# Kernel tuning notes

Measured on AMD Instinct MI355X. Metric: run time of the kernel, lower is better.

The kernel has to match this reference:

```python
import jax, jax.numpy as jnp
import numpy as np

N = 100000   # nodes
E = 800000   # edges per layer
H = 4        # heads
C = 32       # per-head channels (hidden_channels // heads)
IN = 128
HID = H * C  # 128
NEG_SLOPE = 0.2


def gat_layer(x, edge_index, W, att_src, att_dst, bias):
    # PyG GATConv (concat=True, add_self_loops=True)
    n = x.shape[0]
    loop = jnp.arange(n, dtype=edge_index.dtype)
    src = jnp.concatenate([edge_index[0], loop])
    dst = jnp.concatenate([edge_index[1], loop])
    h = (x @ W).reshape(n, H, C)                     # [N,H,C]
    a_src = jnp.sum(h * att_src, axis=-1)            # [N,H]
    a_dst = jnp.sum(h * att_dst, axis=-1)            # [N,H]
    e = jax.nn.leaky_relu(a_src[src] + a_dst[dst], NEG_SLOPE)  # [E',H]
    # segment softmax over incoming edges of each destination node
    m = jax.ops.segment_max(e, dst, num_segments=n)  # [N,H]
    e = jnp.exp(e - m[dst])
    s = jax.ops.segment_sum(e, dst, num_segments=n)  # [N,H]
    alpha = e / (s[dst] + 1e-16)                     # [E',H]
    msg = h[src] * alpha[:, :, None]                 # [E',H,C]
    out = jax.ops.segment_sum(msg, dst, num_segments=n)  # [N,H,C]
    return out.reshape(n, H * C) + bias


def setup_inputs() -> dict:
    key = jax.random.key(0)
    ks = jax.random.split(key, 20)
    inp = {"x": jax.random.normal(ks[0], (N, IN), jnp.float32)}
    dins = [IN, HID, HID]
    for l in range(3):
        din = dins[l]
        inp[f"edge_index{l}"] = jax.random.randint(ks[1 + l], (2, E), 0, N, dtype=jnp.int32)
        inp[f"W{l}"] = jax.random.normal(ks[4 + l], (din, H * C), jnp.float32) / np.sqrt(din)
        inp[f"att_src{l}"] = jax.random.normal(ks[7 + l], (H, C), jnp.float32) * 0.1
        inp[f"att_dst{l}"] = jax.random.normal(ks[10 + l], (H, C), jnp.float32) * 0.1
        inp[f"bias{l}"] = jnp.zeros((H * C,), jnp.float32)
    return inp


def reference(x, edge_index0, edge_index1, edge_index2,
              W0, att_src0, att_dst0, bias0,
              W1, att_src1, att_dst1, bias1,
              W2, att_src2, att_dst2, bias2):
    edges = [edge_index0, edge_index1, edge_index2]
    params = [(W0, att_src0, att_dst0, bias0),
              (W1, att_src1, att_dst1, bias1),
              (W2, att_src2, att_dst2, bias2)]
    for ei, (W, a_s, a_d, b) in zip(edges, params):
        x = jax.nn.relu(gat_layer(x, ei, W, a_s, a_d, b))
    return x
```

## Files before the change

kernel.cpp:

```cpp
#include <hip/hip_runtime.h>
#include <hip/hip_bf16.h>
#include <hip/hip_fp16.h>
#include <type_traits>

#define NNODES 100000
#define NEDGES 800000
#define HIDDIM 128
#define NHEAD 4

#define EPB 8192
#define NBLK 98
#define BSH 7
#define NBUCK 782

typedef _Float16 half8 __attribute__((ext_vector_type(8)));
typedef _Float16 half2t __attribute__((ext_vector_type(2)));
typedef float floatx4 __attribute__((ext_vector_type(4)));


__global__ __launch_bounds__(256) void bucketA_k(const int* __restrict__ e0,
                                                 const int* __restrict__ e1,
                                                 const int* __restrict__ e2,
                                                 int* __restrict__ counts) {
    __shared__ int hist[NBUCK];
    int l = blockIdx.y;
    const int* dst = ((l == 0) ? e0 : (l == 1) ? e1 : e2) + NEDGES;
    int j = blockIdx.x;
    for (int t = threadIdx.x; t < NBUCK; t += 256) hist[t] = 0;
    __syncthreads();
    int base = j * EPB;
    int lim = min(EPB, NEDGES - base);
    for (int i = threadIdx.x; i < lim; i += 256)
        atomicAdd(&hist[dst[base + i] >> BSH], 1);
    __syncthreads();
    int* crow = counts + ((size_t)l * NBLK + j) * NBUCK;
    for (int t = threadIdx.x; t < NBUCK; t += 256) crow[t] = hist[t];
}

__global__ __launch_bounds__(128) void bucketB1_k(int* __restrict__ counts,
                                                  int* __restrict__ bucketTotal) {
    __shared__ int sd[128];
    int b = blockIdx.x, l = blockIdx.y;
    int t = threadIdx.x;
    int v = (t < NBLK) ? counts[((size_t)l * NBLK + t) * NBUCK + b] : 0;
    sd[t] = v;
    __syncthreads();
    for (int off = 1; off < 128; off <<= 1) {
        int u = (t >= off) ? sd[t - off] : 0;
        __syncthreads();
        sd[t] += u;
        __syncthreads();
    }
    if (t < NBLK) counts[((size_t)l * NBLK + t) * NBUCK + b] = sd[t] - v;
    if (t == 127) bucketTotal[l * NBUCK + b] = sd[127];
}

__global__ __launch_bounds__(1024) void bucketB2_k(const int* __restrict__ bucketTotal,
                                                   int* __restrict__ ebBase,
                                                   int* __restrict__ csrBase) {
    __shared__ int sd[1024];
    int l = blockIdx.x;
    int t = threadIdx.x;
    int tot = (t < NBUCK) ? bucketTotal[l * NBUCK + t] : 0;
    sd[t] = tot;
    __syncthreads();
    for (int off = 1; off < 1024; off <<= 1) {
        int u = (t >= off) ? sd[t - off] : 0;
        __syncthreads();
        sd[t] += u;
        __syncthreads();
    }
    if (t < NBUCK) ebBase[l * NBUCK + t] = sd[t] - tot;
    __syncthreads();
    int nb = (t == NBUCK - 1) ? (NNODES - (NBUCK - 1) * 128) : 128;
    int v2 = (t < NBUCK) ? (tot + nb) : 0;
    sd[t] = v2;
    __syncthreads();
    for (int off = 1; off < 1024; off <<= 1) {
        int u = (t >= off) ? sd[t - off] : 0;
        __syncthreads();
        sd[t] += u;
        __syncthreads();
    }
    if (t < NBUCK) csrBase[l * NBUCK + t] = sd[t] - v2;
}

__global__ __launch_bounds__(256) void bucketC_k(const int* __restrict__ e0,
                                                 const int* __restrict__ e1,
                                                 const int* __restrict__ e2,
                                                 const int* __restrict__ counts,
                                                 const int* __restrict__ ebBase,
                                                 int* __restrict__ edgeBuf) {
    __shared__ int cur[NBUCK];
    int l = blockIdx.y;
    const int* ei = (l == 0) ? e0 : (l == 1) ? e1 : e2;
    const int* src = ei;
    const int* dst = ei + NEDGES;
    int j = blockIdx.x;
    const int* bs = counts + ((size_t)l * NBLK + j) * NBUCK;
    const int* eb = ebBase + l * NBUCK;
    for (int t = threadIdx.x; t < NBUCK; t += 256) cur[t] = eb[t] + bs[t];
    __syncthreads();
    int base = j * EPB;
    int lim = min(EPB, NEDGES - base);
    int* ebuf = edgeBuf + (size_t)l * NEDGES;
    for (int i = threadIdx.x; i < lim; i += 256) {
        int d = dst[base + i];
        int s = src[base + i];
        int pos = atomicAdd(&cur[d >> BSH], 1);
        ebuf[pos] = ((d & 127) << 17) | s;
    }
}

__global__ __launch_bounds__(256) void bucketD_k(const int* __restrict__ edgeBuf,
                                                 const int* __restrict__ bucketTotal,
                                                 const int* __restrict__ ebBase,
                                                 const int* __restrict__ csrBase,
                                                 int* __restrict__ offs,
                                                 int* __restrict__ deg,
                                                 int* __restrict__ srcs) {
    __shared__ int cnt[128];
    __shared__ int offl[128];
    __shared__ int cur[128];
    int b = blockIdx.x, l = blockIdx.y;
    int t = threadIdx.x;
    int nb = (b == NBUCK - 1) ? (NNODES - (NBUCK - 1) * 128) : 128;
    int eb0 = ebBase[l * NBUCK + b];
    int ecnt = bucketTotal[l * NBUCK + b];
    int csr0 = csrBase[l * NBUCK + b];
    const int* ebuf = edgeBuf + (size_t)l * NEDGES;
    int* srcsL = srcs + (size_t)l * (NEDGES + NNODES);
    if (t < 128) cnt[t] = 0;
    __syncthreads();
    for (int i = t; i < ecnt; i += 256)
        atomicAdd(&cnt[ebuf[eb0 + i] >> 17], 1);
    __syncthreads();
    if (t < 128) {
        int lane = t & 63;
        int x = cnt[t] + 1;
        #pragma unroll
        for (int o = 1; o < 64; o <<= 1) {
            int u = __shfl_up(x, o);
            if (lane >= o) x += u;
        }
        offl[t] = x;
    }
    __syncthreads();
    if (t < 128) {
        int c = cnt[t];
        int incl = offl[t] + ((t >= 64) ? offl[63] : 0);
        int o = csr0 + incl - (c + 1);
        cur[t] = o;
        if (t < nb) {
            int node = b * 128 + t;
            offs[l * NNODES + node] = o;
            deg[l * NNODES + node] = c;
            srcsL[o + c] = node;
        }
    }
    __syncthreads();
    for (int i = t; i < ecnt; i += 256) {
        int w = ebuf[eb0 + i];
        int pos = atomicAdd(&cur[w >> 17], 1);
        srcsL[pos] = w & 0x1FFFF;
    }
}


template <typename AT>
__global__ __launch_bounds__(256, 2) void gemm_mfma_k(const AT* __restrict__ A,
                                                      const float* __restrict__ B,
                                                      const float* __restrict__ attS,
                                                      const float* __restrict__ attD,
                                                      __half* __restrict__ C16,
                                                      float* __restrict__ aSD, int M) {
    __shared__ __half Bt[144 * 136];
    const int tid = threadIdx.x;
    {
        int kk = (tid & 63) * 2;
        int g = tid >> 6;
        #pragma unroll
        for (int jn = 0; jn < 8; jn++) {
            int n0 = g * 4 + jn * 16;
            float4 r0 = *(const float4*)(B + (size_t)kk * 128 + n0);
            float4 r1 = *(const float4*)(B + (size_t)(kk + 1) * 128 + n0);
            float f0[4] = {r0.x, r0.y, r0.z, r0.w};
            float f1[4] = {r1.x, r1.y, r1.z, r1.w};
            #pragma unroll
            for (int i = 0; i < 4; i++)
                *(__half2*)(&Bt[(n0 + i) * 136 + kk]) = __floats2half2_rn(f0[i], f1[i]);
        }
    }
    if (tid < 128) {
        int k = tid;
        const float* Brow = B + (size_t)k * 128;
        #pragma unroll
        for (int h = 0; h < NHEAD; h++) {
            float s0 = 0.f, s1 = 0.f;
            #pragma unroll 8
            for (int c = 0; c < 32; c++) {
                float bb = Brow[h * 32 + c];
                s0 += bb * attS[h * 32 + c];
                s1 += bb * attD[h * 32 + c];
            }
            Bt[(128 + h * 2 + 0) * 136 + k] = (_Float16)s0;
            Bt[(128 + h * 2 + 1) * 136 + k] = (_Float16)s1;
        }
    } else {
        int k = tid - 128;
        #pragma unroll
        for (int j = 8; j < 16; j++) Bt[(128 + j) * 136 + k] = (_Float16)0.f;
    }
    __syncthreads();

    const int lane = tid & 63;
    const int wave = tid >> 6;
    const int m = lane & 15;
    const int q = lane >> 4;

    half8 bfrag[9][4];
    #pragma unroll
    for (int c = 0; c < 9; c++)
        #pragma unroll
        for (int t = 0; t < 4; t++)
            bfrag[c][t] = *(const half8*)(&Bt[(c * 16 + m) * 136 + t * 32 + q * 8]);

    for (int iter = 0; iter < 4; iter++) {
        int rb = blockIdx.x * 256 + iter * 64 + wave * 16;
        if (rb >= M) break;
        int row = rb + m;
        int rowc = row < M ? row : M - 1;
        half8 a[4];
        if constexpr (std::is_same<AT, __half>::value) {
            const __half* ap = A + (size_t)rowc * HIDDIM;
            #pragma unroll
            for (int t = 0; t < 4; t++)
                a[t] = *(const half8*)(ap + t * 32 + q * 8);
        } else {
            const float* ap = A + (size_t)rowc * HIDDIM;
            #pragma unroll
            for (int t = 0; t < 4; t++) {
                float4 u = *(const float4*)(ap + t * 32 + q * 8);
                float4 v = *(const float4*)(ap + t * 32 + q * 8 + 4);
                half8 h;
                h[0] = (_Float16)u.x; h[1] = (_Float16)u.y;
                h[2] = (_Float16)u.z; h[3] = (_Float16)u.w;
                h[4] = (_Float16)v.x; h[5] = (_Float16)v.y;
                h[6] = (_Float16)v.z; h[7] = (_Float16)v.w;
                a[t] = h;
            }
        }
        floatx4 acc[9];
        #pragma unroll
        for (int c = 0; c < 9; c++) acc[c] = (floatx4){0.f, 0.f, 0.f, 0.f};
        #pragma unroll
        for (int t = 0; t < 4; t++)
            #pragma unroll
            for (int c = 0; c < 9; c++)
                acc[c] = __builtin_amdgcn_mfma_f32_16x16x32_f16(a[t], bfrag[c][t], acc[c], 0, 0, 0);
        #pragma unroll
        for (int c = 0; c < 8; c++)
            #pragma unroll
            for (int r = 0; r < 4; r++) {
                int grow = rb + q * 4 + r;
                if (grow < M)
                    C16[(size_t)grow * HIDDIM + c * 16 + m] = __float2half(acc[c][r]);
            }
        if (m < 8) {
            #pragma unroll
            for (int r = 0; r < 4; r++) {
                int grow = rb + q * 4 + r;
                if (grow < M) aSD[(size_t)grow * 8 + m] = acc[8][r];
            }
        }
    }
}


template <bool HALF_OUT>
__global__ __launch_bounds__(256) void agg_k(const __half* __restrict__ h16,
                                             const int* __restrict__ offs,
                                             const int* __restrict__ deg,
                                             const int* __restrict__ srcs,
                                             const float* __restrict__ aSD,
                                             const float* __restrict__ bias,
                                             void* __restrict__ outv) {
    int tid = threadIdx.x;
    int lane = tid & 63;
    int grp = lane >> 4;
    int cg = lane & 15;
    int c8 = cg * 8;
    int h2 = (cg >> 2) * 2;
    int n = blockIdx.x * 16 + (tid >> 6) * 4 + grp;
    bool nvalid = n < NNODES;
    int nn = nvalid ? n : NNODES - 1;
    int start = offs[nn];
    int cnt = deg[nn] + 1;
    float ad = aSD[(size_t)nn * 8 + h2 + 1];
    half2t acc0[4], acc1[4];
    #pragma unroll
    for (int i = 0; i < 4; i++) {
        acc0[i] = (half2t){(_Float16)0.f, (_Float16)0.f};
        acc1[i] = (half2t){(_Float16)0.f, (_Float16)0.f};
    }
    float wsum = 0.f;
    const int base = grp * 16;

    for (int chunk = 0; chunk < cnt; chunk += 16) {
        int idx = chunk + cg;
        int lim = min(16, cnt - chunk);
        int sv = srcs[start + (idx < cnt ? idx : cnt - 1)];
        int s_a = __shfl(sv, base + 0);
        int s_b = __shfl(sv, base + 1);
        float as_a = aSD[(size_t)s_a * 8 + h2];
        float as_b = aSD[(size_t)s_b * 8 + h2];
        half8 hv_a = *(const half8*)(h16 + (size_t)s_a * HIDDIM + c8);
        half8 hv_b = *(const half8*)(h16 + (size_t)s_b * HIDDIM + c8);
        for (int j = 0; j < lim; j += 2) {
            int j2 = (j + 2 < 16) ? j + 2 : 15;
            int j3 = (j + 3 < 16) ? j + 3 : 15;
            int s_c = __shfl(sv, base + j2);
            int s_d = __shfl(sv, base + j3);
            float as_c = aSD[(size_t)s_c * 8 + h2];
            float as_d = aSD[(size_t)s_d * 8 + h2];
            half8 hv_c = *(const half8*)(h16 + (size_t)s_c * HIDDIM + c8);
            half8 hv_d = *(const half8*)(h16 + (size_t)s_d * HIDDIM + c8);

            float e0 = as_a + ad;
            e0 = (e0 > 0.f) ? e0 : 0.2f * e0;
            float w0 = __expf(e0);
            float e1 = as_b + ad;
            e1 = (e1 > 0.f) ? e1 : 0.2f * e1;
            float w1 = (j + 1 < lim) ? __expf(e1) : 0.f;
            wsum += w0 + w1;
            _Float16 w0h = (_Float16)w0, w1h = (_Float16)w1;
            half2t w02 = (half2t){w0h, w0h}, w12 = (half2t){w1h, w1h};
            #pragma unroll
            for (int i = 0; i < 4; i++) {
                acc0[i] += w02 * (half2t){hv_a[2 * i], hv_a[2 * i + 1]};
                acc1[i] += w12 * (half2t){hv_b[2 * i], hv_b[2 * i + 1]};
            }
            as_a = as_c; as_b = as_d;
            hv_a = hv_c; hv_b = hv_d;
        }
    }

    if (nvalid) {
        float inv = 1.f / (wsum + 1e-16f);
        float v[8];
        #pragma unroll
        for (int i = 0; i < 4; i++) {
            half2t s = acc0[i] + acc1[i];
            float o0 = (float)s[0] * inv + bias[c8 + 2 * i];
            float o1 = (float)s[1] * inv + bias[c8 + 2 * i + 1];
            v[2 * i] = o0 > 0.f ? o0 : 0.f;
            v[2 * i + 1] = o1 > 0.f ? o1 : 0.f;
        }
        if constexpr (HALF_OUT) {
            union { uint4 u; __half2 h2v[4]; } pk;
            #pragma unroll
            for (int i = 0; i < 4; i++) pk.h2v[i] = __floats2half2_rn(v[2 * i], v[2 * i + 1]);
            *(uint4*)((__half*)outv + (size_t)n * HIDDIM + c8) = pk.u;
        } else {
            float* out = (float*)outv;
            *(float4*)(out + (size_t)n * HIDDIM + c8) = make_float4(v[0], v[1], v[2], v[3]);
            *(float4*)(out + (size_t)n * HIDDIM + c8 + 4) = make_float4(v[4], v[5], v[6], v[7]);
        }
    }
}


extern "C" void kernel_launch(void* const* d_in, const int* in_sizes, int n_in,
                              void* d_out, int out_size, void* d_ws, size_t ws_size,
                              hipStream_t stream) {
    (void)in_sizes; (void)n_in; (void)out_size; (void)ws_size;
    const float* x = (const float*)d_in[0];
    const int* e0 = (const int*)d_in[1];
    const int* e1 = (const int*)d_in[6];
    const int* e2 = (const int*)d_in[11];

    char* ws = (char*)d_ws;
    size_t off = 0;
    auto alloc = [&](size_t bytes) -> void* {
        void* p = ws + off;
        off += (bytes + 255) & ~(size_t)255;
        return p;
    };
    __half* xh      = (__half*)alloc((size_t)NNODES * HIDDIM * 2);
    __half* h16     = (__half*)alloc((size_t)NNODES * HIDDIM * 2);
    float* aSD      = (float*)alloc((size_t)NNODES * 8 * 4);
    int* deg        = (int*)alloc((size_t)3 * NNODES * 4);
    int* offsArr    = (int*)alloc((size_t)3 * NNODES * 4);
    int* srcs       = (int*)alloc((size_t)3 * (NEDGES + NNODES) * 4);
    int* counts     = (int*)alloc((size_t)3 * NBLK * NBUCK * 4);
    int* bucketTot  = (int*)alloc((size_t)3 * NBUCK * 4);
    int* ebBase     = (int*)alloc((size_t)3 * NBUCK * 4);
    int* csrBase    = (int*)alloc((size_t)3 * NBUCK * 4);
    int* edgeBuf    = (int*)alloc((size_t)3 * NEDGES * 4);

    hipLaunchKernelGGL(bucketA_k, dim3(NBLK, 3), dim3(256), 0, stream, e0, e1, e2, counts);
    hipLaunchKernelGGL(bucketB1_k, dim3(NBUCK, 3), dim3(128), 0, stream, counts, bucketTot);
    hipLaunchKernelGGL(bucketB2_k, dim3(3), dim3(1024), 0, stream, bucketTot, ebBase, csrBase);
    hipLaunchKernelGGL(bucketC_k, dim3(NBLK, 3), dim3(256), 0, stream,
                       e0, e1, e2, counts, ebBase, edgeBuf);
    hipLaunchKernelGGL(bucketD_k, dim3(NBUCK, 3), dim3(256), 0, stream,
                       edgeBuf, bucketTot, ebBase, csrBase, offsArr, deg, srcs);

    for (int l = 0; l < 3; l++) {
        const float* Wm    = (const float*)d_in[2 + 5 * l];
        const float* attS  = (const float*)d_in[3 + 5 * l];
        const float* attD  = (const float*)d_in[4 + 5 * l];
        const float* biasv = (const float*)d_in[5 + 5 * l];
        const int* offsL = offsArr + l * NNODES;
        const int* degL  = deg + l * NNODES;
        const int* srcsL = srcs + (size_t)l * (NEDGES + NNODES);

        if (l == 0) {
            hipLaunchKernelGGL((gemm_mfma_k<float>), dim3((NNODES + 255) / 256), dim3(256), 0,
                               stream, x, Wm, attS, attD, h16, aSD, NNODES);
        } else {
            hipLaunchKernelGGL((gemm_mfma_k<__half>), dim3((NNODES + 255) / 256), dim3(256), 0,
                               stream, xh, Wm, attS, attD, h16, aSD, NNODES);
        }
        if (l == 2) {
            hipLaunchKernelGGL((agg_k<false>), dim3((NNODES + 15) / 16), dim3(256), 0, stream,
                               h16, offsL, degL, srcsL, aSD, biasv, d_out);
        } else {
            hipLaunchKernelGGL((agg_k<true>), dim3((NNODES + 15) / 16), dim3(256), 0, stream,
                               h16, offsL, degL, srcsL, aSD, biasv, (void*)xh);
        }
    }
}
```

Before: 414.7 us.

## Shrink bucket-sort chunks, rewrite column scan, and remap scatter blocks across XCDs

Cuts the edge chunk per block from 8192 to 2048, giving four times as many blocks for the histogram and scatter passes and more parallelism on a GPU with many CUs. The per-bucket prefix scan over block counts is rewritten so each thread handles one bucket column, split into four wave-sized chunks with a shared-memory carry, replacing the one-block-per-bucket Hillis-Steele scan. The scatter kernel remaps block indices so that consecutive edge chunks are spread across the 8 XCDs, and full chunks use a fully unrolled loop. The costs are a larger counts matrix and more global traffic in the scan, and the remap assumes the block count divides evenly by 8.

Result: faster. 402.5 us (-2.9%).

```diff
diff --git a/kernel.cpp b/kernel.cpp
--- a/kernel.cpp
+++ b/kernel.cpp
@@ -8,8 +8,9 @@
 #define HIDDIM 128
 #define NHEAD 4
 
-#define EPB 8192
-#define NBLK 98
+#define EPB 2048
+#define NBLK 392
+#define XCDG 49
 #define BSH 7
 #define NBUCK 782
 
@@ -30,29 +31,49 @@
     __syncthreads();
     int base = j * EPB;
     int lim = min(EPB, NEDGES - base);
-    for (int i = threadIdx.x; i < lim; i += 256)
-        atomicAdd(&hist[dst[base + i] >> BSH], 1);
+    if (lim == EPB) {
+        #pragma unroll
+        for (int it = 0; it < EPB / 256; it++)
+            atomicAdd(&hist[dst[base + it * 256 + threadIdx.x] >> BSH], 1);
+    } else {
+        for (int i = threadIdx.x; i < lim; i += 256)
+            atomicAdd(&hist[dst[base + i] >> BSH], 1);
+    }
     __syncthreads();
     int* crow = counts + ((size_t)l * NBLK + j) * NBUCK;
     for (int t = threadIdx.x; t < NBUCK; t += 256) crow[t] = hist[t];
 }
 
-__global__ __launch_bounds__(128) void bucketB1_k(int* __restrict__ counts,
+__global__ __launch_bounds__(256) void bucketB1_k(int* __restrict__ counts,
                                                   int* __restrict__ bucketTotal) {
-    __shared__ int sd[128];
-    int b = blockIdx.x, l = blockIdx.y;
-    int t = threadIdx.x;
-    int v = (t < NBLK) ? counts[((size_t)l * NBLK + t) * NBUCK + b] : 0;
-    sd[t] = v;
-    __syncthreads();
-    for (int off = 1; off < 128; off <<= 1) {
-        int u = (t >= off) ? sd[t - off] : 0;
-        __syncthreads();
-        sd[t] += u;
-        __syncthreads();
-    }
-    if (t < NBLK) counts[((size_t)l * NBLK + t) * NBUCK + b] = sd[t] - v;
-    if (t == 127) bucketTotal[l * NBUCK + b] = sd[127];
+    __shared__ int part[4][64];
+    int l = blockIdx.y;
+    int tid = threadIdx.x;
+    int wave = tid >> 6;
+    int lane = tid & 63;
+    int b = blockIdx.x * 64 + lane;
+    bool valid = b < NBUCK;
+    const int CQ = NBLK / 4;
+    int t0 = wave * CQ, t1 = t0 + CQ;
+    int sum = 0;
+    if (valid) {
+        for (int t = t0; t < t1; t++)
+            sum += counts[((size_t)l * NBLK + t) * NBUCK + b];
+    }
+    part[wave][lane] = sum;
+    __syncthreads();
+    int off = 0;
+    for (int w = 0; w < wave; w++) off += part[w][lane];
+    if (valid) {
+        int run = off;
+        for (int t = t0; t < t1; t++) {
+            size_t idx = ((size_t)l * NBLK + t) * NBUCK + b;
+            int v = counts[idx];
+            counts[idx] = run;
+            run += v;
+        }
+        if (wave == 3) bucketTotal[l * NBUCK + b] = run;
+    }
 }
 
 __global__ __launch_bounds__(1024) void bucketB2_k(const int* __restrict__ bucketTotal,
@@ -96,7 +117,8 @@
     const int* ei = (l == 0) ? e0 : (l == 1) ? e1 : e2;
     const int* src = ei;
     const int* dst = ei + NEDGES;
-    int j = blockIdx.x;
+    int bx = blockIdx.x;
+    int j = (bx & 7) * XCDG + (bx >> 3);
     const int* bs = counts + ((size_t)l * NBLK + j) * NBUCK;
     const int* eb = ebBase + l * NBUCK;
     for (int t = threadIdx.x; t < NBUCK; t += 256) cur[t] = eb[t] + bs[t];
@@ -104,11 +126,22 @@
     int base = j * EPB;
     int lim = min(EPB, NEDGES - base);
     int* ebuf = edgeBuf + (size_t)l * NEDGES;
-    for (int i = threadIdx.x; i < lim; i += 256) {
-        int d = dst[base + i];
-        int s = src[base + i];
-        int pos = atomicAdd(&cur[d >> BSH], 1);
-        ebuf[pos] = ((d & 127) << 17) | s;
+    if (lim == EPB) {
+        #pragma unroll
+        for (int it = 0; it < EPB / 256; it++) {
+            int i = it * 256 + threadIdx.x;
+            int d = dst[base + i];
+            int s = src[base + i];
+            int pos = atomicAdd(&cur[d >> BSH], 1);
+            ebuf[pos] = ((d & 127) << 17) | s;
+        }
+    } else {
+        for (int i = threadIdx.x; i < lim; i += 256) {
+            int d = dst[base + i];
+            int s = src[base + i];
+            int pos = atomicAdd(&cur[d >> BSH], 1);
+            ebuf[pos] = ((d & 127) << 17) | s;
+        }
     }
 }
 
@@ -399,7 +432,8 @@
     int* edgeBuf    = (int*)alloc((size_t)3 * NEDGES * 4);
 
     hipLaunchKernelGGL(bucketA_k, dim3(NBLK, 3), dim3(256), 0, stream, e0, e1, e2, counts);
-    hipLaunchKernelGGL(bucketB1_k, dim3(NBUCK, 3), dim3(128), 0, stream, counts, bucketTot);
+    hipLaunchKernelGGL(bucketB1_k, dim3((NBUCK + 63) / 64, 3), dim3(256), 0, stream,
+                       counts, bucketTot);
     hipLaunchKernelGGL(bucketB2_k, dim3(3), dim3(1024), 0, stream, bucketTot, ebBase, csrBase);
     hipLaunchKernelGGL(bucketC_k, dim3(NBLK, 3), dim3(256), 0, stream,
                        e0, e1, e2, counts, ebBase, edgeBuf);
```
